# Kernel tuning notes

Measured on AMD Instinct MI355X. Metric: run time of the kernel, lower is better.

## Reference

```python
import jax, jax.numpy as jnp
import numpy as np


def setup_inputs() -> dict:
    key = jax.random.key(0)
    ks = jax.random.split(key, 12)
    B, N, Dv, E, H, V, T = 128, 196, 512, 512, 1024, 10000, 20
    s = 0.02  # small init scale for numerical stability
    f = lambda k, shp: (jax.random.normal(k, shp, jnp.float32) * s)
    return {
        "features": jax.random.normal(ks[0], (B, N, Dv), jnp.float32),
        "captions": jax.random.randint(ks[1], (B, T), 0, V),
        "W_init_h": f(ks[2], (H, Dv)),
        "W_init_c": f(ks[3], (H, Dv)),
        "W_attn_v": f(ks[4], (1, Dv)),
        "b_attn_v": jnp.zeros((1,), jnp.float32),
        "W_attn_h": f(ks[5], (1, H)),
        "b_attn_h": jnp.zeros((1,), jnp.float32),
        "embed_table": f(ks[6], (V, E)),
        "W_ih": f(ks[7], (4 * H, Dv + E)),
        "W_hh": f(ks[8], (4 * H, H)),
        "b_ih": jnp.zeros((4 * H,), jnp.float32),
        "b_hh": jnp.zeros((4 * H,), jnp.float32),
        "W_out": f(ks[9], (V, H)),
        "b_out": jnp.zeros((V,), jnp.float32),
    }


def reference(features, captions, W_init_h, W_init_c, W_attn_v, b_attn_v,
              W_attn_h, b_attn_h, embed_table, W_ih, W_hh, b_ih, b_hh,
              W_out, b_out):
    B, N, Dv = features.shape
    # _init_hidden: mean over vis_num of linear projections (division by vis_num)
    h0 = jnp.sum(jnp.einsum('bnd,hd->bnh', features, W_init_h), axis=1) / N
    c0 = jnp.sum(jnp.einsum('bnd,hd->bnh', features, W_init_c), axis=1) / N

    emb = embed_table[captions]                      # B,T,E
    emb_t_major = jnp.swapaxes(emb, 0, 1)            # T,B,E
    # visual attention logits are time-invariant; precompute once
    att_v = jnp.einsum('bnd,od->bno', features, W_attn_v) + b_attn_v  # B,N,1

    def step(carry, emb_t):
        h, c = carry
        # soft attention over vis_num locations
        att_h = (h @ W_attn_h.T + b_attn_h)[:, None, :]   # B,1,1
        alpha = jax.nn.softmax(att_v + att_h, axis=1)     # B,N,1
        ctx = jnp.sum(features * alpha, axis=1)           # B,Dv
        # single-step LSTM (PyTorch gate order: i, f, g, o)
        x = jnp.concatenate([ctx, emb_t], axis=-1)        # B,Dv+E
        gates = x @ W_ih.T + h @ W_hh.T + b_ih + b_hh     # B,4H
        i, fg, g, o = jnp.split(gates, 4, axis=-1)
        c_new = jax.nn.sigmoid(fg) * c + jax.nn.sigmoid(i) * jnp.tanh(g)
        h_new = jax.nn.sigmoid(o) * jnp.tanh(c_new)
        words = h_new @ W_out.T + b_out                   # B,V
        return (h_new, c_new), words

    _, word_space = jax.lax.scan(step, (h0, c0), emb_t_major)  # T,B,V
    # pack_padded_sequence with all-equal lengths flattens time-major -> (T*B, V)
    packed = word_space.reshape(-1, word_space.shape[-1])
    return jax.nn.log_softmax(packed, axis=1), jax.nn.softmax(packed, axis=1)
```

## Files before the change

kernel.cpp:

```cpp
#include <hip/hip_runtime.h>
#include <math.h>

#define B    128
#define NLOC 196
#define DV   512
#define EMB  512
#define HD   1024
#define VV   10000
#define TT   20
#define G4   4096
#define VPAD 10112
#define BH   (B*HD)

typedef short bf16x8 __attribute__((ext_vector_type(8)));
typedef short s16x4  __attribute__((ext_vector_type(4)));
typedef float f32x4  __attribute__((ext_vector_type(4)));

__device__ __forceinline__ unsigned short f2bf(float x) {
    unsigned u = __builtin_bit_cast(unsigned, x);
    unsigned r = (u + 0x7fffu + ((u >> 16) & 1u)) >> 16;
    return (unsigned short)r;
}
__device__ __forceinline__ float bf2f(short s) {
    unsigned u = ((unsigned)(unsigned short)s) << 16;
    return __builtin_bit_cast(float, u);
}

__device__ __forceinline__ void gload_lds16(const void* g, void* lds) {
    __builtin_amdgcn_global_load_lds(
        (const __attribute__((address_space(1))) void*)g,
        (__attribute__((address_space(3))) void*)lds, 16, 0, 0);
}


__global__ void attv_kernel(const float* __restrict__ feat, const float* __restrict__ wv,
                            const float* __restrict__ bv, float* __restrict__ attv) {
    int row  = blockIdx.x;
    int lane = threadIdx.x;
    const float* p = feat + (size_t)row * DV;
    float s = 0.f;
    for (int k = lane; k < DV; k += 64) s += p[k] * wv[k];
    for (int off = 32; off > 0; off >>= 1) s += __shfl_down(s, off);
    if (lane == 0) attv[row] = s + bv[0];
}

__global__ void alpha_kernel(const float* __restrict__ attv, float* __restrict__ alpha) {
    int b   = blockIdx.x;
    int tid = threadIdx.x;
    __shared__ float red[256];
    float v = (tid < NLOC) ? attv[b * NLOC + tid] : -1e30f;
    red[tid] = v; __syncthreads();
    for (int s = 128; s > 0; s >>= 1) { if (tid < s) red[tid] = fmaxf(red[tid], red[tid + s]); __syncthreads(); }
    float m = red[0]; __syncthreads();
    float e = (tid < NLOC) ? expf(v - m) : 0.f;
    red[tid] = e; __syncthreads();
    for (int s = 128; s > 0; s >>= 1) { if (tid < s) red[tid] += red[tid + s]; __syncthreads(); }
    float sum = red[0];
    if (tid < NLOC) alpha[b * NLOC + tid] = e / sum;
}

__global__ void fmeanctx_kernel(const float* __restrict__ feat, const float* __restrict__ alpha,
                                short* __restrict__ fmean_b, short* __restrict__ ctx_b) {
    int idx = blockIdx.x * blockDim.x + threadIdx.x;
    if (idx >= B * DV) return;
    int b = idx / DV, d = idx % DV;
    const float* p = feat + (size_t)b * NLOC * DV + d;
    const float* a = alpha + b * NLOC;
    float sm = 0.f, sc = 0.f;
    for (int n = 0; n < NLOC; ++n) {
        float v = p[(size_t)n * DV];
        sm += v;
        sc += a[n] * v;
    }
    fmean_b[idx] = (short)f2bf(sm * (1.0f / NLOC));
    ctx_b[idx]   = (short)f2bf(sc);
}

__global__ void emb_gather_kernel(const int* __restrict__ captions, const float* __restrict__ table,
                                  short* __restrict__ emb_b) {
    size_t q = (size_t)blockIdx.x * blockDim.x + threadIdx.x;
    if (q >= (size_t)TT * B * EMB / 4) return;
    size_t idx = q * 4;
    int k = (int)(idx % EMB);
    int r = (int)(idx / EMB);
    int t = r / B, b = r % B;
    int cap = captions[b * TT + t];
    float4 v = *(const float4*)&table[(size_t)cap * EMB + k];
    s16x4 o = { (short)f2bf(v.x), (short)f2bf(v.y), (short)f2bf(v.z), (short)f2bf(v.w) };
    *(s16x4*)&emb_b[idx] = o;
}

__global__ void f2bf_pad_kernel(const float* __restrict__ in, short* __restrict__ out,
                                size_t n, size_t npad) {
    size_t q = (size_t)blockIdx.x * blockDim.x + threadIdx.x;
    size_t i = q * 4;
    if (i >= npad) return;
    s16x4 o = {0, 0, 0, 0};
    if (i < n) {
        float4 v = *(const float4*)&in[i];
        o = s16x4{ (short)f2bf(v.x), (short)f2bf(v.y), (short)f2bf(v.z), (short)f2bf(v.w) };
    }
    *(s16x4*)&out[i] = o;
}

__global__ void whh_perm_kernel(const float* __restrict__ in, short* __restrict__ out) {
    size_t q = (size_t)blockIdx.x * blockDim.x + threadIdx.x;
    if (q >= (size_t)G4 * HD / 4) return;
    size_t idx = q * 4;
    int k = (int)(idx & (HD - 1));
    int P = (int)(idx >> 10);
    int u = P >> 2, g = P & 3;
    float4 v = *(const float4*)&in[(size_t)(g * HD + u) * HD + k];
    s16x4 o = { (short)f2bf(v.x), (short)f2bf(v.y), (short)f2bf(v.z), (short)f2bf(v.w) };
    *(s16x4*)&out[idx] = o;
}

template<int BN, int WR, int WC, bool BF16OUT>
__global__ __launch_bounds__(256)
void gemm_bf16(const short* __restrict__ A, const short* __restrict__ Bw,
               void* __restrict__ C,
               const float* __restrict__ bias0, const float* __restrict__ bias1,
               int NY, int M, int N, int K, int lda, int ldb, int ldc) {
    constexpr int BM = 128;
    constexpr int BK = 32;
    constexpr int WM = BM / WR;
    constexpr int WN = BN / WC;
    constexpr int FM = WM / 16;
    constexpr int FN = WN / 16;
    __shared__ __align__(16) short As[BM * BK];
    __shared__ __align__(16) short Bs[BN * BK];
    const int tid  = threadIdx.x;
    const int wave = tid >> 6, lane = tid & 63;
    const int wr = wave / WC, wc = wave % WC;

    const int nwg = gridDim.x;
    const int qq = nwg >> 3, rr8 = nwg & 7;
    const int p = blockIdx.x;
    const int xcd = p & 7, slot = p >> 3;
    const int lwg = (xcd < rr8) ? (xcd * (qq + 1) + slot)
                                : (rr8 * (qq + 1) + (xcd - rr8) * qq + slot);
    const int m0 = (lwg % NY) * BM;
    const int n0 = (lwg / NY) * BN;
    const int laneoff = lane * 16;

    f32x4 acc[FM][FN] = {};

    for (int k0 = 0; k0 < K; k0 += BK) {
        #pragma unroll
        for (int r = 0; r < 2; ++r) {
            int o   = r * 4096 + wave * 1024 + laneoff;
            int row = o >> 6;
            int gr  = (o >> 4) & 3;
            int col = ((gr ^ ((row >> 1) & 3)) << 3);
            gload_lds16(A + (size_t)(m0 + row) * lda + k0 + col,
                        (char*)As + r * 4096 + wave * 1024);
        }
        constexpr int BBYTES = BN * BK * 2;
        if constexpr (BBYTES >= 4096) {
            #pragma unroll
            for (int r = 0; r < BBYTES / 4096; ++r) {
                int o   = r * 4096 + wave * 1024 + laneoff;
                int row = o >> 6;
                int gr  = (o >> 4) & 3;
                int col = ((gr ^ ((row >> 1) & 3)) << 3);
                gload_lds16(Bw + (size_t)(n0 + row) * ldb + k0 + col,
                            (char*)Bs + r * 4096 + wave * 1024);
            }
        } else {
            constexpr int NW = BBYTES / 1024;
            if (wave < NW) {
                int o   = wave * 1024 + laneoff;
                int row = o >> 6;
                int gr  = (o >> 4) & 3;
                int col = ((gr ^ ((row >> 1) & 3)) << 3);
                gload_lds16(Bw + (size_t)(n0 + row) * ldb + k0 + col,
                            (char*)Bs + wave * 1024);
            }
        }
        __syncthreads();

        bf16x8 a[FM], b[FN];
        const int kfrg = lane >> 4;
        #pragma unroll
        for (int i = 0; i < FM; ++i) {
            int row = wr * WM + i * 16 + (lane & 15);
            a[i] = *(const bf16x8*)&As[row * BK + ((kfrg ^ ((row >> 1) & 3)) << 3)];
        }
        #pragma unroll
        for (int j = 0; j < FN; ++j) {
            int row = wc * WN + j * 16 + (lane & 15);
            b[j] = *(const bf16x8*)&Bs[row * BK + ((kfrg ^ ((row >> 1) & 3)) << 3)];
        }
        #pragma unroll
        for (int i = 0; i < FM; ++i)
            #pragma unroll
            for (int j = 0; j < FN; ++j)
                acc[i][j] = __builtin_amdgcn_mfma_f32_16x16x32_bf16(a[i], b[j], acc[i][j], 0, 0, 0);
        __syncthreads();
    }

    #pragma unroll
    for (int i = 0; i < FM; ++i) {
        #pragma unroll
        for (int j = 0; j < FN; ++j) {
            int col = n0 + wc * WN + j * 16 + (lane & 15);
            if (col >= N) continue;
            float bv = (bias0 ? bias0[col] : 0.f) + (bias1 ? bias1[col] : 0.f);
            #pragma unroll
            for (int q = 0; q < 4; ++q) {
                int row = m0 + wr * WM + i * 16 + (lane >> 4) * 4 + q;
                if (row < M) {
                    float v = acc[i][j][q] + bv;
                    if constexpr (BF16OUT)
                        ((short*)C)[(size_t)row * ldc + col] = (short)f2bf(v);
                    else
                        ((float*)C)[(size_t)row * ldc + col] = v;
                }
            }
        }
    }
}

__global__ __launch_bounds__(256)
void gemm_k64(const short* __restrict__ A, const short* __restrict__ Bw,
              short* __restrict__ C,
              const float* __restrict__ bias0,
              int NY, int M, int N, int K, int lda, int ldb, int ldc) {
    __shared__ __align__(16) short As[128 * 64];
    __shared__ __align__(16) short Bs[128 * 64];
    const int tid  = threadIdx.x;
    const int wave = tid >> 6, lane = tid & 63;
    const int wr = wave >> 1, wc = wave & 1;

    const int nwg = gridDim.x;
    const int qq = nwg >> 3, rr8 = nwg & 7;
    const int p = blockIdx.x;
    const int xcd = p & 7, slot = p >> 3;
    const int lwg = (xcd < rr8) ? (xcd * (qq + 1) + slot)
                                : (rr8 * (qq + 1) + (xcd - rr8) * qq + slot);
    const int m0 = (lwg % NY) * 128;
    const int n0 = (lwg / NY) * 128;
    const int laneoff = lane * 16;
    const int kfrg = lane >> 4;

    f32x4 acc[4][4] = {};

    for (int k0 = 0; k0 < K; k0 += 64) {
        #pragma unroll
        for (int r = 0; r < 4; ++r) {
            int o   = r * 4096 + wave * 1024 + laneoff;
            int row = o >> 7;
            int gr  = (o >> 4) & 7;
            int col = ((gr ^ (row & 7)) << 3);
            gload_lds16(A + (size_t)(m0 + row) * lda + k0 + col,
                        (char*)As + r * 4096 + wave * 1024);
            gload_lds16(Bw + (size_t)(n0 + row) * ldb + k0 + col,
                        (char*)Bs + r * 4096 + wave * 1024);
        }
        __syncthreads();

        #pragma unroll
        for (int kh = 0; kh < 2; ++kh) {
            bf16x8 a[4], b[4];
            #pragma unroll
            for (int i = 0; i < 4; ++i) {
                int row = wr * 64 + i * 16 + (lane & 15);
                a[i] = *(const bf16x8*)&As[row * 64 + (((kh * 4 + kfrg) ^ (row & 7)) << 3)];
            }
            #pragma unroll
            for (int j = 0; j < 4; ++j) {
                int row = wc * 64 + j * 16 + (lane & 15);
                b[j] = *(const bf16x8*)&Bs[row * 64 + (((kh * 4 + kfrg) ^ (row & 7)) << 3)];
            }
            #pragma unroll
            for (int i = 0; i < 4; ++i)
                #pragma unroll
                for (int j = 0; j < 4; ++j)
                    acc[i][j] = __builtin_amdgcn_mfma_f32_16x16x32_bf16(a[i], b[j], acc[i][j], 0, 0, 0);
        }
        __syncthreads();
    }

    #pragma unroll
    for (int i = 0; i < 4; ++i) {
        #pragma unroll
        for (int j = 0; j < 4; ++j) {
            int col = n0 + wc * 64 + j * 16 + (lane & 15);
            if (col >= N) continue;
            float bv = bias0 ? bias0[col] : 0.f;
            #pragma unroll
            for (int q = 0; q < 4; ++q) {
                int row = m0 + wr * 64 + i * 16 + (lane >> 4) * 4 + q;
                if (row < M) C[(size_t)row * ldc + col] = (short)f2bf(acc[i][j][q] + bv);
            }
        }
    }
}

__global__ __launch_bounds__(256)
void lstm_step8(const short* __restrict__ Hprev, const short* __restrict__ Whh_p,
                const short* __restrict__ pre_t, const short* __restrict__ gctx_b,
                float* __restrict__ cbuf, short* __restrict__ Hnext,
                short* __restrict__ Hall_t) {
    __shared__ __align__(16) short As[32 * 256];
    __shared__ __align__(16) short Ws[32 * 256];
    __shared__ float gsm[4][32][8];
    const int tid  = threadIdx.x;
    const int lane = tid & 63, wave = tid >> 6;
    const int n0 = blockIdx.x * 32;
    const int m0 = blockIdx.y * 32;

    const int mi = wave >> 1, ni = wave & 1;
    const int arowL = mi * 16 + (lane & 15);
    const int browL = ni * 16 + (lane & 15);
    const int kg    = lane >> 4;

    f32x4 acc = {};

    for (int qk = 0; qk < 4; ++qk) {
        const int k0 = qk * 256;
        #pragma unroll
        for (int it = 0; it < 4; ++it) {
            int fg  = it * 256 + tid;
            int row = fg >> 5;
            int g   = fg & 31;
            int col = (g ^ (row & 7)) * 8;
            gload_lds16(Hprev + (size_t)(m0 + row) * HD + k0 + col,
                        (char*)As + it * 4096 + wave * 1024);
            gload_lds16(Whh_p + (size_t)(n0 + row) * HD + k0 + col,
                        (char*)Ws + it * 4096 + wave * 1024);
        }
        __syncthreads();
        #pragma unroll
        for (int ks = 0; ks < 8; ++ks) {
            int lg = ks * 4 + kg;
            bf16x8 a = *(const bf16x8*)((const char*)As + arowL * 512 + ((lg ^ (arowL & 7)) << 4));
            bf16x8 w = *(const bf16x8*)((const char*)Ws + browL * 512 + ((lg ^ (browL & 7)) << 4));
            acc = __builtin_amdgcn_mfma_f32_16x16x32_bf16(a, w, acc, 0, 0, 0);
        }
        __syncthreads();
    }

    #pragma unroll
    for (int q = 0; q < 4; ++q) {
        int rr = mi * 16 + (lane >> 4) * 4 + q;
        gsm[browL & 3][rr][browL >> 2] = acc[q];
    }
    __syncthreads();

    const int m = tid >> 3, u8 = tid & 7;
    const int r = m0 + m, u = blockIdx.x * 8 + u8;
    size_t pb = (size_t)r * G4 + u;
    float gi  = gsm[0][m][u8] + bf2f(pre_t[pb])          + bf2f(gctx_b[pb]);
    float gf  = gsm[1][m][u8] + bf2f(pre_t[pb + HD])     + bf2f(gctx_b[pb + HD]);
    float gg2 = gsm[2][m][u8] + bf2f(pre_t[pb + 2 * HD]) + bf2f(gctx_b[pb + 2 * HD]);
    float go  = gsm[3][m][u8] + bf2f(pre_t[pb + 3 * HD]) + bf2f(gctx_b[pb + 3 * HD]);
    float si = 1.f / (1.f + expf(-gi));
    float sf = 1.f / (1.f + expf(-gf));
    float so = 1.f / (1.f + expf(-go));
    float cn = sf * cbuf[(size_t)r * HD + u] + si * tanhf(gg2);
    float hn = so * tanhf(cn);
    cbuf[(size_t)r * HD + u] = cn;
    short hb = (short)f2bf(hn);
    Hnext[(size_t)r * HD + u]  = hb;
    Hall_t[(size_t)r * HD + u] = hb;
}

__global__ __launch_bounds__(512)
void softmax_kernel(const short* __restrict__ wbf, float* __restrict__ logout,
                    float* __restrict__ smout) {
    __shared__ float rowbuf[VV];
    __shared__ float red[512];
    int r = blockIdx.x;
    int tid = threadIdx.x;
    const short* row = wbf + (size_t)r * VV;
    float m = -1e30f;
    for (int i = tid; i < VV; i += 512) {
        float v = bf2f(row[i]);
        rowbuf[i] = v;
        m = fmaxf(m, v);
    }
    red[tid] = m; __syncthreads();
    for (int s = 256; s > 0; s >>= 1) { if (tid < s) red[tid] = fmaxf(red[tid], red[tid + s]); __syncthreads(); }
    m = red[0]; __syncthreads();
    float sum = 0.f;
    for (int i = tid; i < VV; i += 512) sum += expf(rowbuf[i] - m);
    red[tid] = sum; __syncthreads();
    for (int s = 256; s > 0; s >>= 1) { if (tid < s) red[tid] += red[tid + s]; __syncthreads(); }
    sum = red[0];
    float inv = 1.f / sum;
    float lz = logf(sum);
    for (int i = tid; i < VV; i += 512) {
        float x = rowbuf[i];
        smout[(size_t)r * VV + i]  = expf(x - m) * inv;
        logout[(size_t)r * VV + i] = x - m - lz;
    }
}

extern "C" void kernel_launch(void* const* d_in, const int* in_sizes, int n_in,
                              void* d_out, int out_size, void* d_ws, size_t ws_size,
                              hipStream_t stream) {
    const float* features    = (const float*)d_in[0];
    const int*   captions    = (const int*)  d_in[1];
    const float* W_init_h    = (const float*)d_in[2];
    const float* W_init_c    = (const float*)d_in[3];
    const float* W_attn_v    = (const float*)d_in[4];
    const float* b_attn_v    = (const float*)d_in[5];
    const float* embed_table = (const float*)d_in[8];
    const float* W_ih        = (const float*)d_in[9];
    const float* W_hh        = (const float*)d_in[10];
    const float* b_ih        = (const float*)d_in[11];
    const float* b_hh        = (const float*)d_in[12];
    const float* W_out       = (const float*)d_in[13];
    const float* b_out       = (const float*)d_in[14];

    float* out   = (float*)d_out;
    float* words = out;
    float* s2    = out + (size_t)TT * B * VV;

    short* gate_pre_b = (short*)s2;
    short* Hall_b   = (short*)(s2 + (size_t)10485760);
    short* Wout_b   = (short*)(s2 + (size_t)10485760 + 1310720);
    short* Wih_b    = Wout_b + (size_t)VPAD * HD;
    short* Whh_b    = Wih_b  + (size_t)G4 * HD;
    short* Wini_h_b = Whh_b  + (size_t)G4 * HD;
    short* Wini_c_b = Wini_h_b + (size_t)HD * DV;

    char* w = (char*)d_ws;
    size_t off = 0;
    auto alloc = [&](size_t bytes) { void* p = w + off; off = (off + bytes + 255) & ~255UL; return p; };
    float* attv   = (float*)alloc((size_t)B * NLOC * 4);
    float* alpha  = (float*)alloc((size_t)B * NLOC * 4);
    short* gctx_b = (short*)alloc((size_t)B * G4 * 2);
    float* cbuf   = (float*)alloc((size_t)B * HD * 4);
    short* fmean_b= (short*)alloc((size_t)B * DV * 2);
    short* ctx_b  = (short*)alloc((size_t)B * DV * 2);
    short* h_ping = (short*)alloc((size_t)B * HD * 2);
    short* h_pong = (short*)alloc((size_t)B * HD * 2);
    short* emb_b  = (short*)alloc((size_t)TT * B * EMB * 2);
    short* words_bf = (short*)alloc((size_t)TT * B * VV * 2);

    f2bf_pad_kernel<<<((size_t)VPAD * HD / 4 + 255) / 256, 256, 0, stream>>>(
        W_out, Wout_b, (size_t)VV * HD, (size_t)VPAD * HD);
    f2bf_pad_kernel<<<((size_t)G4 * HD / 4 + 255) / 256, 256, 0, stream>>>(
        W_ih, Wih_b, (size_t)G4 * HD, (size_t)G4 * HD);
    whh_perm_kernel<<<((size_t)G4 * HD / 4 + 255) / 256, 256, 0, stream>>>(W_hh, Whh_b);
    f2bf_pad_kernel<<<((size_t)HD * DV / 4 + 255) / 256, 256, 0, stream>>>(
        W_init_h, Wini_h_b, (size_t)HD * DV, (size_t)HD * DV);
    f2bf_pad_kernel<<<((size_t)HD * DV / 4 + 255) / 256, 256, 0, stream>>>(
        W_init_c, Wini_c_b, (size_t)HD * DV, (size_t)HD * DV);

    attv_kernel<<<B * NLOC, 64, 0, stream>>>(features, W_attn_v, b_attn_v, attv);
    alpha_kernel<<<B, 256, 0, stream>>>(attv, alpha);
    fmeanctx_kernel<<<(B * DV + 255) / 256, 256, 0, stream>>>(features, alpha, fmean_b, ctx_b);
    emb_gather_kernel<<<((size_t)TT * B * EMB / 4 + 255) / 256, 256, 0, stream>>>(
        captions, embed_table, emb_b);

    gemm_bf16<32, 4, 1, true><<<dim3(HD / 32), 256, 0, stream>>>(
        fmean_b, Wini_h_b, h_ping, nullptr, nullptr, 1, B, HD, DV, DV, DV, HD);
    gemm_bf16<32, 4, 1, false><<<dim3(HD / 32), 256, 0, stream>>>(
        fmean_b, Wini_c_b, cbuf, nullptr, nullptr, 1, B, HD, DV, DV, DV, HD);

    gemm_bf16<32, 4, 1, true><<<dim3(G4 / 32), 256, 0, stream>>>(
        ctx_b, Wih_b, gctx_b, b_ih, b_hh, 1, B, G4, DV, DV, HD, G4);
    gemm_k64<<<dim3((G4 / 128) * (TT * B / 128)), 256, 0, stream>>>(
        emb_b, Wih_b + DV, gate_pre_b, nullptr, TT * B / 128,
        TT * B, G4, EMB, EMB, DV + EMB, G4);

    for (int t = 0; t < TT; ++t) {
        lstm_step8<<<dim3(G4 / 32, B / 32), 256, 0, stream>>>(
            (t & 1) ? h_pong : h_ping, Whh_b, gate_pre_b + (size_t)t * B * G4, gctx_b,
            cbuf, (t & 1) ? h_ping : h_pong, Hall_b + (size_t)t * BH);
    }

    gemm_k64<<<dim3((VPAD / 128) * (TT * B / 128)), 256, 0, stream>>>(
        Hall_b, Wout_b, words_bf, b_out, TT * B / 128,
        TT * B, VV, HD, HD, HD, VV);
    softmax_kernel<<<TT * B, 512, 0, stream>>>(words_bf, words, s2);
}
```

Measured before the change: 454.3 us.

## Merge weight conversions into one launch, widen LSTM K-tile, drop h ping-pong

Folds the five weight-conversion launches into a single kernel that branches on the global thread index. Doubles the LSTM step's K-tile to 512, so it does two load/sync rounds instead of four, at the cost of twice the shared memory per block. It also drops the separate hidden-state ping-pong buffers: each step reads the previous step's slice of the all-steps hidden buffer, removing one redundant store per element. These cut launch overhead and barrier count, but the larger shared-memory footprint may reduce occupancy.

```diff
diff --git a/kernel.cpp b/kernel.cpp
--- a/kernel.cpp
+++ b/kernel.cpp
@@ -90,29 +90,62 @@
     *(s16x4*)&emb_b[idx] = o;
 }
 
-__global__ void f2bf_pad_kernel(const float* __restrict__ in, short* __restrict__ out,
-                                size_t n, size_t npad) {
+#define N_WOUT ((size_t)VPAD * HD / 4)
+#define N_WIH  ((size_t)G4 * HD / 4)
+#define N_WHH  ((size_t)G4 * HD / 4)
+#define N_WINI ((size_t)HD * DV / 4)
+__global__ void convert_all_kernel(const float* __restrict__ W_out, short* __restrict__ Wout_b,
+                                   const float* __restrict__ W_ih,  short* __restrict__ Wih_b,
+                                   const float* __restrict__ W_hh,  short* __restrict__ Whh_b,
+                                   const float* __restrict__ W_ini_h, short* __restrict__ Wini_h_b,
+                                   const float* __restrict__ W_ini_c, short* __restrict__ Wini_c_b) {
     size_t q = (size_t)blockIdx.x * blockDim.x + threadIdx.x;
-    size_t i = q * 4;
-    if (i >= npad) return;
-    s16x4 o = {0, 0, 0, 0};
-    if (i < n) {
-        float4 v = *(const float4*)&in[i];
-        o = s16x4{ (short)f2bf(v.x), (short)f2bf(v.y), (short)f2bf(v.z), (short)f2bf(v.w) };
-    }
-    *(s16x4*)&out[i] = o;
-}
-
-__global__ void whh_perm_kernel(const float* __restrict__ in, short* __restrict__ out) {
-    size_t q = (size_t)blockIdx.x * blockDim.x + threadIdx.x;
-    if (q >= (size_t)G4 * HD / 4) return;
-    size_t idx = q * 4;
-    int k = (int)(idx & (HD - 1));
-    int P = (int)(idx >> 10);
-    int u = P >> 2, g = P & 3;
-    float4 v = *(const float4*)&in[(size_t)(g * HD + u) * HD + k];
-    s16x4 o = { (short)f2bf(v.x), (short)f2bf(v.y), (short)f2bf(v.z), (short)f2bf(v.w) };
-    *(s16x4*)&out[idx] = o;
+    const float* src; short* dst; size_t idx;
+    if (q < N_WOUT) {
+        idx = q * 4;
+        size_t n = (size_t)VV * HD;
+        s16x4 o = {0, 0, 0, 0};
+        if (idx < n) {
+            float4 v = *(const float4*)&W_out[idx];
+            o = s16x4{ (short)f2bf(v.x), (short)f2bf(v.y), (short)f2bf(v.z), (short)f2bf(v.w) };
+        }
+        *(s16x4*)&Wout_b[idx] = o;
+        return;
+    }
+    q -= N_WOUT;
+    if (q < N_WIH) {
+        idx = q * 4;
+        float4 v = *(const float4*)&W_ih[idx];
+        s16x4 o = { (short)f2bf(v.x), (short)f2bf(v.y), (short)f2bf(v.z), (short)f2bf(v.w) };
+        *(s16x4*)&Wih_b[idx] = o;
+        return;
+    }
+    q -= N_WIH;
+    if (q < N_WHH) {
+        idx = q * 4;
+        int k = (int)(idx & (HD - 1));
+        int P = (int)(idx >> 10);
+        int u = P >> 2, g = P & 3;
+        float4 v = *(const float4*)&W_hh[(size_t)(g * HD + u) * HD + k];
+        s16x4 o = { (short)f2bf(v.x), (short)f2bf(v.y), (short)f2bf(v.z), (short)f2bf(v.w) };
+        *(s16x4*)&Whh_b[idx] = o;
+        return;
+    }
+    q -= N_WHH;
+    if (q < N_WINI) {
+        idx = q * 4;
+        float4 v = *(const float4*)&W_ini_h[idx];
+        s16x4 o = { (short)f2bf(v.x), (short)f2bf(v.y), (short)f2bf(v.z), (short)f2bf(v.w) };
+        *(s16x4*)&Wini_h_b[idx] = o;
+        return;
+    }
+    q -= N_WINI;
+    if (q < N_WINI) {
+        idx = q * 4;
+        float4 v = *(const float4*)&W_ini_c[idx];
+        s16x4 o = { (short)f2bf(v.x), (short)f2bf(v.y), (short)f2bf(v.z), (short)f2bf(v.w) };
+        *(s16x4*)&Wini_c_b[idx] = o;
+    }
 }
 
 template<int BN, int WR, int WC, bool BF16OUT>
@@ -298,12 +331,11 @@
 }
 
 __global__ __launch_bounds__(256)
-void lstm_step8(const short* __restrict__ Hprev, const short* __restrict__ Whh_p,
+void lstm_step9(const short* __restrict__ Hprev, const short* __restrict__ Whh_p,
                 const short* __restrict__ pre_t, const short* __restrict__ gctx_b,
-                float* __restrict__ cbuf, short* __restrict__ Hnext,
-                short* __restrict__ Hall_t) {
-    __shared__ __align__(16) short As[32 * 256];
-    __shared__ __align__(16) short Ws[32 * 256];
+                float* __restrict__ cbuf, short* __restrict__ Hall_t) {
+    __shared__ __align__(16) short As[32 * 512];
+    __shared__ __align__(16) short Ws[32 * 512];
     __shared__ float gsm[4][32][8];
     const int tid  = threadIdx.x;
     const int lane = tid & 63, wave = tid >> 6;
@@ -317,13 +349,13 @@
 
     f32x4 acc = {};
 
-    for (int qk = 0; qk < 4; ++qk) {
-        const int k0 = qk * 256;
-        #pragma unroll
-        for (int it = 0; it < 4; ++it) {
+    for (int h2 = 0; h2 < 2; ++h2) {
+        const int k0 = h2 * 512;
+        #pragma unroll
+        for (int it = 0; it < 8; ++it) {
             int fg  = it * 256 + tid;
-            int row = fg >> 5;
-            int g   = fg & 31;
+            int row = fg >> 6;
+            int g   = fg & 63;
             int col = (g ^ (row & 7)) * 8;
             gload_lds16(Hprev + (size_t)(m0 + row) * HD + k0 + col,
                         (char*)As + it * 4096 + wave * 1024);
@@ -332,10 +364,10 @@
         }
         __syncthreads();
         #pragma unroll
-        for (int ks = 0; ks < 8; ++ks) {
+        for (int ks = 0; ks < 16; ++ks) {
             int lg = ks * 4 + kg;
-            bf16x8 a = *(const bf16x8*)((const char*)As + arowL * 512 + ((lg ^ (arowL & 7)) << 4));
-            bf16x8 w = *(const bf16x8*)((const char*)Ws + browL * 512 + ((lg ^ (browL & 7)) << 4));
+            bf16x8 a = *(const bf16x8*)((const char*)As + arowL * 1024 + ((lg ^ (arowL & 7)) << 4));
+            bf16x8 w = *(const bf16x8*)((const char*)Ws + browL * 1024 + ((lg ^ (browL & 7)) << 4));
             acc = __builtin_amdgcn_mfma_f32_16x16x32_bf16(a, w, acc, 0, 0, 0);
         }
         __syncthreads();
@@ -361,9 +393,7 @@
     float cn = sf * cbuf[(size_t)r * HD + u] + si * tanhf(gg2);
     float hn = so * tanhf(cn);
     cbuf[(size_t)r * HD + u] = cn;
-    short hb = (short)f2bf(hn);
-    Hnext[(size_t)r * HD + u]  = hb;
-    Hall_t[(size_t)r * HD + u] = hb;
+    Hall_t[(size_t)r * HD + u] = (short)f2bf(hn);
 }
 
 __global__ __launch_bounds__(512)
@@ -435,20 +465,16 @@
     float* cbuf   = (float*)alloc((size_t)B * HD * 4);
     short* fmean_b= (short*)alloc((size_t)B * DV * 2);
     short* ctx_b  = (short*)alloc((size_t)B * DV * 2);
-    short* h_ping = (short*)alloc((size_t)B * HD * 2);
-    short* h_pong = (short*)alloc((size_t)B * HD * 2);
+    short* h0_b   = (short*)alloc((size_t)B * HD * 2);
     short* emb_b  = (short*)alloc((size_t)TT * B * EMB * 2);
     short* words_bf = (short*)alloc((size_t)TT * B * VV * 2);
 
-    f2bf_pad_kernel<<<((size_t)VPAD * HD / 4 + 255) / 256, 256, 0, stream>>>(
-        W_out, Wout_b, (size_t)VV * HD, (size_t)VPAD * HD);
-    f2bf_pad_kernel<<<((size_t)G4 * HD / 4 + 255) / 256, 256, 0, stream>>>(
-        W_ih, Wih_b, (size_t)G4 * HD, (size_t)G4 * HD);
-    whh_perm_kernel<<<((size_t)G4 * HD / 4 + 255) / 256, 256, 0, stream>>>(W_hh, Whh_b);
-    f2bf_pad_kernel<<<((size_t)HD * DV / 4 + 255) / 256, 256, 0, stream>>>(
-        W_init_h, Wini_h_b, (size_t)HD * DV, (size_t)HD * DV);
-    f2bf_pad_kernel<<<((size_t)HD * DV / 4 + 255) / 256, 256, 0, stream>>>(
-        W_init_c, Wini_c_b, (size_t)HD * DV, (size_t)HD * DV);
+    {
+        size_t total = N_WOUT + N_WIH + N_WHH + 2 * N_WINI;
+        convert_all_kernel<<<(total + 255) / 256, 256, 0, stream>>>(
+            W_out, Wout_b, W_ih, Wih_b, W_hh, Whh_b,
+            W_init_h, Wini_h_b, W_init_c, Wini_c_b);
+    }
 
     attv_kernel<<<B * NLOC, 64, 0, stream>>>(features, W_attn_v, b_attn_v, attv);
     alpha_kernel<<<B, 256, 0, stream>>>(attv, alpha);
@@ -457,7 +483,7 @@
         captions, embed_table, emb_b);
 
     gemm_bf16<32, 4, 1, true><<<dim3(HD / 32), 256, 0, stream>>>(
-        fmean_b, Wini_h_b, h_ping, nullptr, nullptr, 1, B, HD, DV, DV, DV, HD);
+        fmean_b, Wini_h_b, h0_b, nullptr, nullptr, 1, B, HD, DV, DV, DV, HD);
     gemm_bf16<32, 4, 1, false><<<dim3(HD / 32), 256, 0, stream>>>(
         fmean_b, Wini_c_b, cbuf, nullptr, nullptr, 1, B, HD, DV, DV, DV, HD);
 
@@ -468,9 +494,10 @@
         TT * B, G4, EMB, EMB, DV + EMB, G4);
 
     for (int t = 0; t < TT; ++t) {
-        lstm_step8<<<dim3(G4 / 32, B / 32), 256, 0, stream>>>(
-            (t & 1) ? h_pong : h_ping, Whh_b, gate_pre_b + (size_t)t * B * G4, gctx_b,
-            cbuf, (t & 1) ? h_ping : h_pong, Hall_b + (size_t)t * BH);
+        const short* Hprev = (t == 0) ? h0_b : (Hall_b + (size_t)(t - 1) * BH);
+        lstm_step9<<<dim3(G4 / 32, B / 32), 256, 0, stream>>>(
+            Hprev, Whh_b, gate_pre_b + (size_t)t * B * G4, gctx_b,
+            cbuf, Hall_b + (size_t)t * BH);
     }
 
     gemm_k64<<<dim3((VPAD / 128) * (TT * B / 128)), 256, 0, stream>>>(
```

After: 437.8 us. 3.6% less time.
